# Performance work log

Measured on AMD Instinct MI355X. Metric: run time of the kernel, lower is better.

Reference implementation:

```python
import jax, jax.numpy as jnp
import numpy as np

LN_EPS = 1e-5

# Per-tensor symmetric fake-quant (brevitas-style):
#  - activations: signed int8, non-narrow range [-128, 127], scale = absmax / 128
#  - weights:     signed int8, narrow range     [-127, 127], scale = absmax / 127

def _fake_quant(v, qmin, qmax, denom):
    s = jnp.max(jnp.abs(v)) / denom
    s = jnp.maximum(s, jnp.asarray(1e-12, v.dtype))
    q = jnp.clip(jnp.round(v / s), qmin, qmax)
    return q * s

def fq_act(v):
    return _fake_quant(v, -128.0, 127.0, 128.0)

def fq_weight(w):
    return _fake_quant(w, -127.0, 127.0, 127.0)

def layer_norm(x, gamma, beta):
    mu = jnp.mean(x, axis=-1, keepdims=True)
    var = jnp.mean(jnp.square(x - mu), axis=-1, keepdims=True)
    return (x - mu) * jax.lax.rsqrt(var + LN_EPS) * gamma + beta


def setup_inputs() -> dict:
    key = jax.random.key(0)
    k_x, k_w1, k_w2 = jax.random.split(key, 3)
    B, T, D, H = 16, 4096, 768, 3072
    x = jax.random.normal(k_x, (B, T, D), dtype=jnp.float32)
    gamma = jnp.ones((D,), jnp.float32)
    beta = jnp.zeros((D,), jnp.float32)
    W1 = jax.random.normal(k_w1, (H, D), dtype=jnp.float32) * (1.0 / np.sqrt(D))
    b1 = jnp.zeros((H,), jnp.float32)
    W2 = jax.random.normal(k_w2, (D, H), dtype=jnp.float32) * (1.0 / np.sqrt(H))
    b2 = jnp.zeros((D,), jnp.float32)
    return {"x": x, "gamma": gamma, "beta": beta, "W1": W1, "b1": b1, "W2": W2, "b2": b2}


def reference(x, gamma, beta, W1, b1, W2, b2):
    xn = layer_norm(x, gamma, beta)
    # fc1: quantize input + weight per-tensor, GEMM, float bias add
    h = jnp.einsum('btd,hd->bth', fq_act(xn), fq_weight(W1)) + b1
    h = jax.nn.gelu(h, approximate=False)  # nn.GELU default = exact erf
    # dropout p=0 -> identity
    out = jnp.einsum('bth,dh->btd', fq_act(h), fq_weight(W2)) + b2
    return out
```

## Files before the change

kernel.cpp:

```cpp
#include <hip/hip_runtime.h>
#include <math.h>


typedef __attribute__((ext_vector_type(4))) float  f4;
typedef __attribute__((ext_vector_type(4))) int    i32x4;
typedef __attribute__((ext_vector_type(4))) unsigned char  uc4;
typedef __attribute__((ext_vector_type(4))) unsigned int   u4;

__device__ __forceinline__ unsigned short f2bf_rn(float f) {
    unsigned u = __float_as_uint(f);
    u += 0x7FFFu + ((u >> 16) & 1u);
    return (unsigned short)(u >> 16);
}

template <int NW>
__device__ __forceinline__ void block_atomic_max(float v, unsigned* slot,
                                                 float* red, int tid) {
    int lane = tid & 63, wv = tid >> 6;
    #pragma unroll
    for (int m = 32; m; m >>= 1) v = fmaxf(v, __shfl_xor(v, m));
    if (lane == 0) red[wv] = v;
    __syncthreads();
    if (tid == 0) {
        float r = red[0];
        #pragma unroll
        for (int i = 1; i < NW; i++) r = fmaxf(r, red[i]);
        atomicMax(slot, __float_as_uint(r));
    }
}

__device__ __forceinline__ void gll16(const void* g, void* l) {
    __builtin_amdgcn_global_load_lds(
        (const __attribute__((address_space(1))) void*)g,
        (__attribute__((address_space(3))) void*)l, 16, 0, 0);
}

__device__ __forceinline__ void ln_row(const f4* xr, int lane, f4 v[3],
                                       float& mu, float& rs) {
    float s = 0.f;
    #pragma unroll
    for (int c = 0; c < 3; c++) {
        v[c] = xr[lane + 64 * c];
        s += v[c][0] + v[c][1] + v[c][2] + v[c][3];
    }
    #pragma unroll
    for (int m = 1; m < 64; m <<= 1) s += __shfl_xor(s, m);
    mu = s * (1.0f / 768.0f);
    float q = 0.f;
    #pragma unroll
    for (int c = 0; c < 3; c++) {
        #pragma unroll
        for (int k = 0; k < 4; k++) { float d = v[c][k] - mu; q += d * d; }
    }
    #pragma unroll
    for (int m = 1; m < 64; m <<= 1) q += __shfl_xor(q, m);
    rs = rsqrtf(q * (1.0f / 768.0f) + 1e-5f);
}

__global__ __launch_bounds__(256) void ln_absmax_kernel(
        const float* __restrict__ x, const float* __restrict__ gamma,
        const float* __restrict__ beta, unsigned* __restrict__ slot, long NR) {
    __shared__ float red[4];
    int tid = threadIdx.x, lane = tid & 63, wv = tid >> 6;
    const f4* g4 = (const f4*)gamma;
    const f4* b4 = (const f4*)beta;
    long rstep = (long)gridDim.x * 4;
    float wmax = 0.f;
    for (long row = (long)blockIdx.x * 4 + wv; row < NR; row += rstep) {
        const f4* xr = (const f4*)(x + row * 768);
        f4 v[3]; float mu, rs;
        ln_row(xr, lane, v, mu, rs);
        #pragma unroll
        for (int c = 0; c < 3; c++) {
            f4 g = g4[lane + 64 * c], b = b4[lane + 64 * c];
            #pragma unroll
            for (int k = 0; k < 4; k++) {
                float xn = (v[c][k] - mu) * rs * g[k] + b[k];
                wmax = fmaxf(wmax, fabsf(xn));
            }
        }
    }
    block_atomic_max<4>(wmax, slot, red, tid);
}

__global__ __launch_bounds__(256) void ln_quant_kernel(
        const float* __restrict__ x, const float* __restrict__ gamma,
        const float* __restrict__ beta, unsigned char* __restrict__ qx,
        const unsigned* __restrict__ amax_bits, long NR) {
    int tid = threadIdx.x, lane = tid & 63, wv = tid >> 6;
    long row = (long)blockIdx.x * 4 + wv;
    if (row >= NR) return;
    float sx = fmaxf(__uint_as_float(*amax_bits) * (1.0f / 128.0f), 1e-12f);
    const f4* xr = (const f4*)(x + row * 768);
    const f4* g4 = (const f4*)gamma;
    const f4* b4 = (const f4*)beta;
    f4 v[3]; float mu, rs;
    ln_row(xr, lane, v, mu, rs);
    uc4* qr = (uc4*)(qx + row * 768);
    #pragma unroll
    for (int c = 0; c < 3; c++) {
        f4 g = g4[lane + 64 * c], b = b4[lane + 64 * c];
        uc4 o;
        #pragma unroll
        for (int k = 0; k < 4; k++) {
            float xn = (v[c][k] - mu) * rs * g[k] + b[k];
            float q = fminf(fmaxf(rintf(xn / sx), -128.0f), 127.0f);
            o[k] = (unsigned char)(int)q;
        }
        qr[lane + 64 * c] = o;
    }
}

__global__ __launch_bounds__(256) void absmax_kernel(
        const float* __restrict__ w, long n4, unsigned* __restrict__ slot) {
    __shared__ float red[4];
    int tid = threadIdx.x;
    long stride = (long)gridDim.x * 256;
    float mx = 0.f;
    for (long i = (long)blockIdx.x * 256 + tid; i < n4; i += stride) {
        f4 v = ((const f4*)w)[i];
        mx = fmaxf(mx, fmaxf(fmaxf(fabsf(v[0]), fabsf(v[1])),
                             fmaxf(fabsf(v[2]), fabsf(v[3]))));
    }
    block_atomic_max<4>(mx, slot, red, tid);
}

__global__ __launch_bounds__(256) void quant_w_kernel(
        const float* __restrict__ w, unsigned char* __restrict__ qw, long n4,
        const unsigned* __restrict__ amax_bits) {
    long i = (long)blockIdx.x * 256 + threadIdx.x;
    if (i >= n4) return;
    float s = fmaxf(__uint_as_float(*amax_bits) * (1.0f / 127.0f), 1e-12f);
    f4 v = ((const f4*)w)[i];
    uc4 o;
    #pragma unroll
    for (int k = 0; k < 4; k++) {
        float q = fminf(fmaxf(rintf(v[k] / s), -127.0f), 127.0f);
        o[k] = (unsigned char)(int)q;
    }
    ((uc4*)qw)[i] = o;
}

__global__ __launch_bounds__(256) void quant_h_kernel(
        unsigned int* __restrict__ h, const unsigned* __restrict__ amax_bits,
        long n32) {
    long i = (long)blockIdx.x * 256 + threadIdx.x;
    if (i >= n32) return;
    float s = fmaxf(__uint_as_float(*amax_bits) * (1.0f / 128.0f), 1e-12f);
    u4 d0 = ((const u4*)h)[2 * i];
    u4 d1 = ((const u4*)h)[2 * i + 1];
    u4 o;
    #pragma unroll
    for (int w = 0; w < 4; w++) {
        unsigned r = 0;
        #pragma unroll
        for (int j = 0; j < 2; j++) {
            unsigned dw = (w < 2) ? d0[(w & 1) * 2 + j] : d1[(w & 1) * 2 + j];
            float lo = __uint_as_float(dw << 16);
            float hi = __uint_as_float(dw & 0xFFFF0000u);
            int qa = (int)fminf(fmaxf(rintf(lo / s), -128.0f), 127.0f);
            int qb = (int)fminf(fmaxf(rintf(hi / s), -128.0f), 127.0f);
            r |= ((unsigned)(unsigned char)qa) << (16 * j);
            r |= ((unsigned)(unsigned char)qb) << (16 * j + 8);
        }
        o[w] = r;
    }
    ((u4*)h)[2 * i] = o;
}

#define AB(b,kh) ((b)*65536 + (kh)*16384)
#define BB(b,kh) ((b)*65536 + 32768 + (kh)*16384)
#define STA(p, eo, rb) gll16(gA[p] + (long)(eo) * GAP, lds + (rb) + ldst[p])
#define STB(p, eo, rb) gll16(gB[p] + (eo), lds + (rb) + ldst[p])
#define VMC(n) asm volatile("s_waitcnt vmcnt(" #n ")" ::: "memory")

#define PHASE(BUF, KS, MB, STAGE, TAIL) do {                                  \
    i32x4 aF[4];                                                              \
    _Pragma("unroll")                                                         \
    for (int m_ = 0; m_ < 4; m_++)                                            \
      aF[m_] = *(const i32x4*)(lds + AB(BUF,KS) + aoff + (MB + m_) * 1024);   \
    if (MB == 0) {                                                            \
      _Pragma("unroll")                                                       \
      for (int n_ = 0; n_ < 4; n_++)                                          \
        bF[n_] = *(const i32x4*)(lds + BB(BUF,KS) + boff + n_ * 1024);        \
    }                                                                         \
    STAGE                                                                     \
    __builtin_amdgcn_s_barrier();                                             \
    asm volatile("s_waitcnt lgkmcnt(0)" ::: "memory");                        \
    __builtin_amdgcn_s_setprio(1);                                            \
    _Pragma("unroll")                                                         \
    for (int m_ = 0; m_ < 4; m_++)                                            \
      _Pragma("unroll")                                                       \
      for (int n_ = 0; n_ < 4; n_++)                                          \
        acc[MB + m_][n_] = __builtin_amdgcn_mfma_i32_16x16x64_i8(             \
            aF[m_], bF[n_], acc[MB + m_][n_], 0, 0, 0);                       \
    __builtin_amdgcn_s_setprio(0);                                            \
    TAIL                                                                      \
    __builtin_amdgcn_s_barrier();                                             \
  } while (0)

template <int GAP, int EPI>
__global__ __launch_bounds__(512, 2) void gemm256i(
        const unsigned char* __restrict__ A, const unsigned char* __restrict__ B,
        int K, const unsigned* __restrict__ amaxA_bits,
        const unsigned* __restrict__ amaxB_bits, const float* __restrict__ bias,
        void* __restrict__ Cout, int ldc, unsigned* __restrict__ amax_out) {
    __shared__ __align__(16) char lds[131072];
    __shared__ float red[8];
    int tid = threadIdx.x, lane = tid & 63, wv = tid >> 6;
    int wm = wv >> 2, wn = wv & 3;

    int nwg = gridDim.x * gridDim.y;
    int flat = blockIdx.y * gridDim.x + blockIdx.x;
    int swz = (flat & 7) * (nwg >> 3) + (flat >> 3);
    int ncol = gridDim.x;
    long rowBase = (long)(swz / ncol) * 256;
    long colBase = (long)(swz % ncol) * 256;

    i32x4 acc[8][4] = {};
    i32x4 bF[4];

    int rl = lane & 15, cq = lane >> 4;
    int roff = rl * 64 + ((cq ^ ((rl >> 1) & 3)) * 16);
    int aoff = wm * 8192 + roff;
    int boff = wn * 4096 + roff;

    const unsigned char* gA[2]; const unsigned char* gB[2]; int ldst[2];
    #pragma unroll
    for (int p = 0; p < 2; p++) {
        int s = p * 512 + tid;
        int r = s >> 2;
        int gc = (s & 3) ^ ((r >> 1) & 3);
        gA[p] = A + (rowBase + r) * (long)K * GAP + gc * 16 * GAP;
        gB[p] = B + (colBase + r) * (long)K + gc * 16;
        ldst[p] = s * 16;
    }

    #pragma unroll
    for (int p = 0; p < 2; p++) {
        STA(p, 0,   AB(0,0));
        STA(p, 64,  AB(0,1));
        STB(p, 0,   BB(0,0));
        STB(p, 64,  BB(0,1));
    }
    #pragma unroll
    for (int p = 0; p < 2; p++) {
        STA(p, 128, AB(1,0));
        STB(p, 128, BB(1,0));
    }
    VMC(4);
    __builtin_amdgcn_s_barrier();

    const int nit = (K >> 8) - 1;
    for (int i = 0; i < nit; i++) {
        PHASE(0,0,0, { STA(0,192,AB(1,1)); STA(1,192,AB(1,1)); }, );
        PHASE(0,0,4, { STB(0,192,BB(1,1)); STB(1,192,BB(1,1)); }, );
        PHASE(0,1,0, { STA(0,256,AB(0,0)); STA(1,256,AB(0,0)); }, );
        PHASE(0,1,4, { STB(0,256,BB(0,0)); STB(1,256,BB(0,0)); }, VMC(4); );
        PHASE(1,0,0, { STA(0,320,AB(0,1)); STA(1,320,AB(0,1)); }, );
        PHASE(1,0,4, { STB(0,320,BB(0,1)); STB(1,320,BB(0,1)); }, );
        PHASE(1,1,0, { STA(0,384,AB(1,0)); STA(1,384,AB(1,0)); }, );
        PHASE(1,1,4, { STB(0,384,BB(1,0)); STB(1,384,BB(1,0)); }, VMC(4); );
        gA[0] += 256 * GAP; gA[1] += 256 * GAP; gB[0] += 256; gB[1] += 256;
    }
    PHASE(0,0,0, { STA(0,192,AB(1,1)); STA(1,192,AB(1,1)); }, );
    PHASE(0,0,4, { STB(0,192,BB(1,1)); STB(1,192,BB(1,1)); }, );
    PHASE(0,1,0, { }, );
    PHASE(0,1,4, { }, VMC(0); );
    PHASE(1,0,0, { }, );
    PHASE(1,0,4, { }, );
    PHASE(1,1,0, { }, );
    PHASE(1,1,4, { }, );

    float sA = fmaxf(__uint_as_float(*amaxA_bits) * (1.0f / 128.0f), 1e-12f);
    float sB = fmaxf(__uint_as_float(*amaxB_bits) * (1.0f / 127.0f), 1e-12f);
    float sAB = sA * sB;
    int cr = cq * 4;
    int cc = rl;

    float bv[4];
    #pragma unroll
    for (int n = 0; n < 4; n++) bv[n] = bias[colBase + wn * 64 + n * 16 + cc];

    if (EPI == 0) {
        unsigned short* Hm = (unsigned short*)Cout;
        float mx = 0.f;
        #pragma unroll
        for (int m = 0; m < 8; m++) {
            #pragma unroll
            for (int r = 0; r < 4; r++) {
                long ro = (rowBase + wm * 128 + m * 16 + cr + r) * (long)ldc
                          + colBase + wn * 64 + cc;
                #pragma unroll
                for (int n = 0; n < 4; n++) {
                    float v = (float)acc[m][n][r] * sAB + bv[n];
                    float g = 0.5f * v * (1.0f + erff(v * 0.70710678118654752f));
                    mx = fmaxf(mx, fabsf(g));
                    Hm[ro + n * 16] = f2bf_rn(g);
                }
            }
        }
        block_atomic_max<8>(mx, amax_out, red, tid);
    } else {
        float* O = (float*)Cout;
        #pragma unroll
        for (int m = 0; m < 8; m++) {
            #pragma unroll
            for (int r = 0; r < 4; r++) {
                long ro = (rowBase + wm * 128 + m * 16 + cr + r) * (long)ldc
                          + colBase + wn * 64 + cc;
                #pragma unroll
                for (int n = 0; n < 4; n++)
                    O[ro + n * 16] = (float)acc[m][n][r] * sAB + bv[n];
            }
        }
    }
}

extern "C" void kernel_launch(void* const* d_in, const int* in_sizes, int n_in,
                              void* d_out, int out_size, void* d_ws, size_t ws_size,
                              hipStream_t stream) {
    const float* x     = (const float*)d_in[0];
    const float* gamma = (const float*)d_in[1];
    const float* beta  = (const float*)d_in[2];
    const float* W1    = (const float*)d_in[3];
    const float* b1    = (const float*)d_in[4];
    const float* W2    = (const float*)d_in[5];
    const float* b2    = (const float*)d_in[6];
    float* out = (float*)d_out;

    const int  D  = in_sizes[1];
    const int  H  = in_sizes[4];
    const long NR = (long)in_sizes[0] / D;

    char* ws = (char*)d_ws;
    unsigned* amax = (unsigned*)ws;
    unsigned char* qx  = (unsigned char*)(ws + 256);
    unsigned char* qw1 = qx  + (size_t)NR * D;
    unsigned char* qw2 = qw1 + (size_t)H * D;
    unsigned short* hq = (unsigned short*)(qw2 + (size_t)H * D);

    hipMemsetAsync(amax, 0, 16, stream);

    long wn4 = (long)H * D / 4;
    absmax_kernel<<<1024, 256, 0, stream>>>(W1, wn4, amax + 1);
    absmax_kernel<<<1024, 256, 0, stream>>>(W2, wn4, amax + 2);
    ln_absmax_kernel<<<2048, 256, 0, stream>>>(x, gamma, beta, amax + 0, NR);

    quant_w_kernel<<<(unsigned)((wn4 + 255) / 256), 256, 0, stream>>>(W1, qw1, wn4, amax + 1);
    quant_w_kernel<<<(unsigned)((wn4 + 255) / 256), 256, 0, stream>>>(W2, qw2, wn4, amax + 2);
    ln_quant_kernel<<<(unsigned)(NR / 4), 256, 0, stream>>>(x, gamma, beta, qx, amax + 0, NR);

    dim3 g1(H / 256, (unsigned)(NR / 256));
    gemm256i<1, 0><<<g1, 512, 0, stream>>>(qx, qw1, D, amax + 0, amax + 1, b1,
                                           (void*)hq, H, amax + 3);

    long n32 = NR * (long)H / 16;
    quant_h_kernel<<<(unsigned)((n32 + 255) / 256), 256, 0, stream>>>(
        (unsigned int*)hq, amax + 3, n32);

    dim3 g2(D / 256, (unsigned)(NR / 256));
    gemm256i<2, 1><<<g2, 512, 0, stream>>>((const unsigned char*)hq, qw2, H,
                                           amax + 3, amax + 2, b2,
                                           (void*)out, D, nullptr);
}
```

Baseline: 1.169 ms.

## Merge half-tile GEMM phases into full k-slice phases with fewer barriers

Restructures the int8 MFMA main loop so each phase loads all 8 A fragments and 4 B fragments for a 64-wide k-slice and issues 32 MFMAs, instead of splitting into two half phases of 16 MFMAs. A and B global-to-LDS loads for a slice are issued together, and vmcnt waits are adjusted per phase. This halves the number of barrier pairs per iteration, cutting sync overhead, at the cost of more live fragment registers and coarser interleaving of loads with compute.

```diff
diff --git a/kernel.cpp b/kernel.cpp
--- a/kernel.cpp
+++ b/kernel.cpp
@@ -170,30 +170,31 @@
 
 #define AB(b,kh) ((b)*65536 + (kh)*16384)
 #define BB(b,kh) ((b)*65536 + 32768 + (kh)*16384)
-#define STA(p, eo, rb) gll16(gA[p] + (long)(eo) * GAP, lds + (rb) + ldst[p])
-#define STB(p, eo, rb) gll16(gB[p] + (eo), lds + (rb) + ldst[p])
 #define VMC(n) asm volatile("s_waitcnt vmcnt(" #n ")" ::: "memory")
-
-#define PHASE(BUF, KS, MB, STAGE, TAIL) do {                                  \
-    i32x4 aF[4];                                                              \
+#define SK(eo, rbA, rbB) {                                                    \
+    gll16(gA[0] + (long)(eo) * GAP, lds + (rbA) + ldst[0]);                   \
+    gll16(gA[1] + (long)(eo) * GAP, lds + (rbA) + ldst[1]);                   \
+    gll16(gB[0] + (eo),             lds + (rbB) + ldst[0]);                   \
+    gll16(gB[1] + (eo),             lds + (rbB) + ldst[1]); }
+
+#define PHASE2(BUF, KS, STAGE, TAIL) do {                                     \
+    i32x4 aF[8]; i32x4 bF[4];                                                 \
     _Pragma("unroll")                                                         \
-    for (int m_ = 0; m_ < 4; m_++)                                            \
-      aF[m_] = *(const i32x4*)(lds + AB(BUF,KS) + aoff + (MB + m_) * 1024);   \
-    if (MB == 0) {                                                            \
-      _Pragma("unroll")                                                       \
-      for (int n_ = 0; n_ < 4; n_++)                                          \
-        bF[n_] = *(const i32x4*)(lds + BB(BUF,KS) + boff + n_ * 1024);        \
-    }                                                                         \
+    for (int m_ = 0; m_ < 8; m_++)                                            \
+      aF[m_] = *(const i32x4*)(lds + AB(BUF,KS) + aoff + m_ * 1024);          \
+    _Pragma("unroll")                                                         \
+    for (int n_ = 0; n_ < 4; n_++)                                            \
+      bF[n_] = *(const i32x4*)(lds + BB(BUF,KS) + boff + n_ * 1024);          \
     STAGE                                                                     \
     __builtin_amdgcn_s_barrier();                                             \
     asm volatile("s_waitcnt lgkmcnt(0)" ::: "memory");                        \
     __builtin_amdgcn_s_setprio(1);                                            \
     _Pragma("unroll")                                                         \
-    for (int m_ = 0; m_ < 4; m_++)                                            \
+    for (int m_ = 0; m_ < 8; m_++)                                            \
       _Pragma("unroll")                                                       \
       for (int n_ = 0; n_ < 4; n_++)                                          \
-        acc[MB + m_][n_] = __builtin_amdgcn_mfma_i32_16x16x64_i8(             \
-            aF[m_], bF[n_], acc[MB + m_][n_], 0, 0, 0);                       \
+        acc[m_][n_] = __builtin_amdgcn_mfma_i32_16x16x64_i8(                  \
+            aF[m_], bF[n_], acc[m_][n_], 0, 0, 0);                            \
     __builtin_amdgcn_s_setprio(0);                                            \
     TAIL                                                                      \
     __builtin_amdgcn_s_barrier();                                             \
@@ -218,7 +219,6 @@
     long colBase = (long)(swz % ncol) * 256;
 
     i32x4 acc[8][4] = {};
-    i32x4 bF[4];
 
     int rl = lane & 15, cq = lane >> 4;
     int roff = rl * 64 + ((cq ^ ((rl >> 1) & 3)) * 16);
@@ -236,41 +236,24 @@
         ldst[p] = s * 16;
     }
 
-    #pragma unroll
-    for (int p = 0; p < 2; p++) {
-        STA(p, 0,   AB(0,0));
-        STA(p, 64,  AB(0,1));
-        STB(p, 0,   BB(0,0));
-        STB(p, 64,  BB(0,1));
-    }
-    #pragma unroll
-    for (int p = 0; p < 2; p++) {
-        STA(p, 128, AB(1,0));
-        STB(p, 128, BB(1,0));
-    }
-    VMC(4);
+    SK(0,   AB(0,0), BB(0,0));
+    SK(64,  AB(0,1), BB(0,1));
+    SK(128, AB(1,0), BB(1,0));
+    VMC(8);
     __builtin_amdgcn_s_barrier();
 
     const int nit = (K >> 8) - 1;
     for (int i = 0; i < nit; i++) {
-        PHASE(0,0,0, { STA(0,192,AB(1,1)); STA(1,192,AB(1,1)); }, );
-        PHASE(0,0,4, { STB(0,192,BB(1,1)); STB(1,192,BB(1,1)); }, );
-        PHASE(0,1,0, { STA(0,256,AB(0,0)); STA(1,256,AB(0,0)); }, );
-        PHASE(0,1,4, { STB(0,256,BB(0,0)); STB(1,256,BB(0,0)); }, VMC(4); );
-        PHASE(1,0,0, { STA(0,320,AB(0,1)); STA(1,320,AB(0,1)); }, );
-        PHASE(1,0,4, { STB(0,320,BB(0,1)); STB(1,320,BB(0,1)); }, );
-        PHASE(1,1,0, { STA(0,384,AB(1,0)); STA(1,384,AB(1,0)); }, );
-        PHASE(1,1,4, { STB(0,384,BB(1,0)); STB(1,384,BB(1,0)); }, VMC(4); );
+        PHASE2(0,0, SK(192, AB(1,1), BB(1,1)), VMC(8); );
+        PHASE2(0,1, SK(256, AB(0,0), BB(0,0)), VMC(8); );
+        PHASE2(1,0, SK(320, AB(0,1), BB(0,1)), VMC(8); );
+        PHASE2(1,1, SK(384, AB(1,0), BB(1,0)), VMC(8); );
         gA[0] += 256 * GAP; gA[1] += 256 * GAP; gB[0] += 256; gB[1] += 256;
     }
-    PHASE(0,0,0, { STA(0,192,AB(1,1)); STA(1,192,AB(1,1)); }, );
-    PHASE(0,0,4, { STB(0,192,BB(1,1)); STB(1,192,BB(1,1)); }, );
-    PHASE(0,1,0, { }, );
-    PHASE(0,1,4, { }, VMC(0); );
-    PHASE(1,0,0, { }, );
-    PHASE(1,0,4, { }, );
-    PHASE(1,1,0, { }, );
-    PHASE(1,1,4, { }, );
+    PHASE2(0,0, SK(192, AB(1,1), BB(1,1)), VMC(8); );
+    PHASE2(0,1, { },                       VMC(4); );
+    PHASE2(1,0, { },                       VMC(0); );
+    PHASE2(1,1, { },                               );
 
     float sA = fmaxf(__uint_as_float(*amaxA_bits) * (1.0f / 128.0f), 1e-12f);
     float sB = fmaxf(__uint_as_float(*amaxB_bits) * (1.0f / 127.0f), 1e-12f);
```

After: 1.201 ms. 2.7% more time.
